# Kernel optimization log

Measured on AMD Instinct MI355X. Metric: run time of the kernel, lower is better.

## Reference

```python
import jax, jax.numpy as jnp
import numpy as np

N = 50000
E = 800000
D_IN = 128
D_OUT = 128
LN_EPS = 1e-5
DROP_P = 0.1


def setup_inputs() -> dict:
    key = jax.random.key(0)
    ks = jax.random.split(key, 8)
    x = jax.random.normal(ks[0], (N, D_IN), dtype=jnp.float32)
    edge_index = jax.random.randint(ks[1], (2, E), 0, N, dtype=jnp.int64)
    # dropout mask: binary keep-mask scaled by 1/(1-p), as torch dropout produces
    u = jax.random.uniform(ks[2], (N, D_IN), dtype=jnp.float32)
    dropout_mask = (u > DROP_P).astype(jnp.float32) / (1.0 - DROP_P)
    # LayerNorm affine params
    gamma = jnp.ones((D_IN,), dtype=jnp.float32)
    beta = jnp.zeros((D_IN,), dtype=jnp.float32)
    # SAGEConv linears: lin_l (aggregated neighbors, with bias), lin_r (root, no bias)
    s = 1.0 / np.sqrt(D_IN)
    w_l = jax.random.uniform(ks[3], (D_OUT, D_IN), minval=-s, maxval=s, dtype=jnp.float32)
    b_l = jax.random.uniform(ks[4], (D_OUT,), minval=-s, maxval=s, dtype=jnp.float32)
    w_r = jax.random.uniform(ks[5], (D_OUT, D_IN), minval=-s, maxval=s, dtype=jnp.float32)
    return {"x": x, "edge_index": edge_index, "dropout_mask": dropout_mask,
            "gamma": gamma, "beta": beta, "w_l": w_l, "b_l": b_l, "w_r": w_r}


def reference(x, edge_index, dropout_mask, gamma, beta, w_l, b_l, w_r):
    # LayerNorm + ReLU + dropout mask
    mu = jnp.mean(x, axis=-1, keepdims=True)
    var = jnp.mean(jnp.square(x - mu), axis=-1, keepdims=True)
    h = (x - mu) * jax.lax.rsqrt(var + LN_EPS) * gamma + beta
    h = jax.nn.relu(h) * dropout_mask  # [N, D_IN]
    # SAGEConv: mean-aggregate source features into target nodes
    src = edge_index[0]
    dst = edge_index[1]
    msg = h[src]  # [E, D_IN] gathered messages
    agg = jax.ops.segment_sum(msg, dst, num_segments=N)  # [N, D_IN]
    deg = jax.ops.segment_sum(jnp.ones((E,), dtype=h.dtype), dst, num_segments=N)
    agg = agg / jnp.maximum(deg, 1.0)[:, None]
    # out = lin_l(agg) + lin_r(h)
    out = agg @ w_l.T + b_l + h @ w_r.T  # [N, D_OUT]
    return out
```

## Files before the change

### kernel.cpp

```cpp
#include <hip/hip_runtime.h>
#include <hip/hip_bf16.h>

#define N_NODES 50000
#define N_EDGES 800000
#define D 128
#define NB_PREP ((N_NODES + 255) / 256)
#define NB_GEMM ((N_NODES + 63) / 64)
#define EDGES_PER_GEMM_BLOCK 1024
#define CAP 64

typedef short bf16x8 __attribute__((ext_vector_type(8)));
typedef float f32x4 __attribute__((ext_vector_type(4)));

__device__ __forceinline__ unsigned int bf16u(float f) {
  __hip_bfloat16 b = __float2bfloat16(f);
  return (unsigned int)*reinterpret_cast<unsigned short*>(&b);
}

__global__ __launch_bounds__(256) void prep_kernel(
    const float* __restrict__ w_l, const float* __restrict__ w_r,
    unsigned int* __restrict__ wb, int* __restrict__ deg) {
  const int i = blockIdx.x * 256 + threadIdx.x;
  if (i < N_NODES) deg[i] = 0;
  if (i < 4096) {
    const int fid = i >> 6;
    const int l = i & 63;
    const int lm = l & 15;
    const int quad = l >> 4;
    const int sub = fid >> 2;
    const int ch = fid & 3;
    const float* srcw = (sub < 8) ? (w_l + (size_t)(sub * 16 + lm) * D)
                                  : (w_r + (size_t)((sub - 8) * 16 + lm) * D);
    const float4 a = *(const float4*)(srcw + ch * 32 + quad * 8);
    const float4 b = *(const float4*)(srcw + ch * 32 + quad * 8 + 4);
    uint4 v;
    v.x = (bf16u(a.y) << 16) | bf16u(a.x);
    v.y = (bf16u(a.w) << 16) | bf16u(a.z);
    v.z = (bf16u(b.y) << 16) | bf16u(b.x);
    v.w = (bf16u(b.w) << 16) | bf16u(b.z);
    ((uint4*)wb)[(size_t)fid * 64 + l] = v;
  }
}

__global__ __launch_bounds__(256, 4) void gemm_kernel(
    const float* __restrict__ x, const float* __restrict__ mask,
    const float* __restrict__ gamma, const float* __restrict__ beta,
    const unsigned int* __restrict__ wb, const float* __restrict__ b_l,
    unsigned int* __restrict__ gb, float* __restrict__ rp,
    const int* __restrict__ ei, int* __restrict__ deg,
    unsigned short* __restrict__ bucket) {
  const int t = threadIdx.x;
  const int w = t >> 6;
  const int l = t & 63;
  const int lm = l & 15;
  const int quad = l >> 4;
  const int nb = blockIdx.x * 64;

  const int e = blockIdx.x * EDGES_PER_GEMM_BLOCK + t * 4;
  const bool efull = (e + 3 < N_EDGES);
  int4 d4, s4, r4;
  if (efull) {
    d4 = *(const int4*)(ei + N_EDGES + e);
    s4 = *(const int4*)(ei + e);
    r4.x = atomicAdd(&deg[d4.x], 1);
    r4.y = atomicAdd(&deg[d4.y], 1);
    r4.z = atomicAdd(&deg[d4.z], 1);
    r4.w = atomicAdd(&deg[d4.w], 1);
  } else {
    for (int k = e; k < N_EDGES; ++k) {
      const int dst = ei[N_EDGES + k];
      const int r = atomicAdd(&deg[dst], 1);
      if (r < CAP) bucket[(size_t)dst * CAP + r] = (unsigned short)ei[k];
    }
  }

  int anode = nb + w * 16 + lm;
  if (anode >= N_NODES) anode = N_NODES - 1;
  const float* xrow = x + (size_t)anode * D;
  float xv[32];
  float s = 0.f, q = 0.f;
#pragma unroll
  for (int ch = 0; ch < 4; ++ch) {
    const float4 a = *(const float4*)(xrow + ch * 32 + quad * 8);
    const float4 b = *(const float4*)(xrow + ch * 32 + quad * 8 + 4);
    xv[ch * 8 + 0] = a.x; xv[ch * 8 + 1] = a.y;
    xv[ch * 8 + 2] = a.z; xv[ch * 8 + 3] = a.w;
    xv[ch * 8 + 4] = b.x; xv[ch * 8 + 5] = b.y;
    xv[ch * 8 + 6] = b.z; xv[ch * 8 + 7] = b.w;
    s += (a.x + a.y) + (a.z + a.w) + (b.x + b.y) + (b.z + b.w);
    q += a.x * a.x + a.y * a.y + a.z * a.z + a.w * a.w +
         b.x * b.x + b.y * b.y + b.z * b.z + b.w * b.w;
  }
  s += __shfl_xor(s, 16);
  s += __shfl_xor(s, 32);
  q += __shfl_xor(q, 16);
  q += __shfl_xor(q, 32);
  const float mean = s * (1.0f / 128.0f);
  const float var = q * (1.0f / 128.0f) - mean * mean;
  const float rs = rsqrtf(var + 1e-5f);

  const float* mrow = mask + (size_t)anode * D;
  bf16x8 af[4];
#pragma unroll
  for (int ch = 0; ch < 4; ++ch) {
    const int c0 = ch * 32 + quad * 8;
    const float4 g0 = *(const float4*)(gamma + c0);
    const float4 g1 = *(const float4*)(gamma + c0 + 4);
    const float4 b0 = *(const float4*)(beta + c0);
    const float4 b1 = *(const float4*)(beta + c0 + 4);
    const float4 m0 = *(const float4*)(mrow + c0);
    const float4 m1 = *(const float4*)(mrow + c0 + 4);
    const float gv[8] = {g0.x, g0.y, g0.z, g0.w, g1.x, g1.y, g1.z, g1.w};
    const float bv[8] = {b0.x, b0.y, b0.z, b0.w, b1.x, b1.y, b1.z, b1.w};
    const float mv[8] = {m0.x, m0.y, m0.z, m0.w, m1.x, m1.y, m1.z, m1.w};
#pragma unroll
    for (int j = 0; j < 8; ++j) {
      const float hv =
          fmaxf((xv[ch * 8 + j] - mean) * rs * gv[j] + bv[j], 0.0f) * mv[j];
      af[ch][j] = (short)bf16u(hv);
    }
  }

  if (efull) {
    if (r4.x < CAP) bucket[(size_t)d4.x * CAP + r4.x] = (unsigned short)s4.x;
    if (r4.y < CAP) bucket[(size_t)d4.y * CAP + r4.y] = (unsigned short)s4.y;
    if (r4.z < CAP) bucket[(size_t)d4.z * CAP + r4.z] = (unsigned short)s4.z;
    if (r4.w < CAP) bucket[(size_t)d4.w * CAP + r4.w] = (unsigned short)s4.w;
  }

  f32x4 acc[16];
#pragma unroll
  for (int sub = 0; sub < 16; ++sub) acc[sub] = (f32x4){0.f, 0.f, 0.f, 0.f};
  const bf16x8* BsF = (const bf16x8*)wb;
#pragma unroll
  for (int sub = 0; sub < 16; ++sub)
#pragma unroll
    for (int ch = 0; ch < 4; ++ch)
      acc[sub] = __builtin_amdgcn_mfma_f32_16x16x32_bf16(
          af[ch], BsF[(sub * 4 + ch) * 64 + l], acc[sub], 0, 0, 0);

  float blv[8];
#pragma unroll
  for (int j = 0; j < 8; ++j) blv[j] = b_l[j * 16 + lm];

  const int node0 = nb + w * 16 + quad * 4;
#pragma unroll
  for (int reg = 0; reg < 4; ++reg) {
    const int node = node0 + reg;
    if (node < N_NODES) {
      uint4 p;
      p.x = (bf16u(acc[1][reg]) << 16) | bf16u(acc[0][reg]);
      p.y = (bf16u(acc[3][reg]) << 16) | bf16u(acc[2][reg]);
      p.z = (bf16u(acc[5][reg]) << 16) | bf16u(acc[4][reg]);
      p.w = (bf16u(acc[7][reg]) << 16) | bf16u(acc[6][reg]);
      ((uint4*)gb)[(size_t)node * 16 + lm] = p;
      float4 q0, q1;
      q0.x = acc[8][reg] + blv[0];
      q0.y = acc[9][reg] + blv[1];
      q0.z = acc[10][reg] + blv[2];
      q0.w = acc[11][reg] + blv[3];
      q1.x = acc[12][reg] + blv[4];
      q1.y = acc[13][reg] + blv[5];
      q1.z = acc[14][reg] + blv[6];
      q1.w = acc[15][reg] + blv[7];
      ((float4*)rp)[(size_t)node * 32 + lm * 2 + 0] = q0;
      ((float4*)rp)[(size_t)node * 32 + lm * 2 + 1] = q1;
    }
  }
}

#define ACC8(v)                                     \
  do {                                              \
    acc[0] += __uint_as_float((v).x << 16);         \
    acc[1] += __uint_as_float((v).x & 0xffff0000u); \
    acc[2] += __uint_as_float((v).y << 16);         \
    acc[3] += __uint_as_float((v).y & 0xffff0000u); \
    acc[4] += __uint_as_float((v).z << 16);         \
    acc[5] += __uint_as_float((v).z & 0xffff0000u); \
    acc[6] += __uint_as_float((v).w << 16);         \
    acc[7] += __uint_as_float((v).w & 0xffff0000u); \
  } while (0)

__global__ __launch_bounds__(256) void agg_kernel(
    const int* __restrict__ deg, const unsigned short* __restrict__ bucket,
    const unsigned int* __restrict__ gb, const float* __restrict__ rp,
    float* __restrict__ out) {
  const int l = threadIdx.x & 63;
  const int q = l >> 4;
  const int c = l & 15;
  const int n = blockIdx.x * 4 + (threadIdx.x >> 6);
  const int dg = deg[n];
  const int cnt = min(dg, CAP);
  const uint4* g4 = (const uint4*)gb;
  float acc[8];
#pragma unroll
  for (int k = 0; k < 8; ++k) acc[k] = 0.0f;
  int idx = (l < cnt) ? (int)bucket[(size_t)n * CAP + l] : 0;
  int j = 0;
  for (; j + 16 <= cnt; j += 16) {
    const int i0 = __shfl(idx, j + 0 + q);
    const int i1 = __shfl(idx, j + 4 + q);
    const int i2 = __shfl(idx, j + 8 + q);
    const int i3 = __shfl(idx, j + 12 + q);
    const uint4 v0 = g4[(size_t)i0 * 16 + c];
    const uint4 v1 = g4[(size_t)i1 * 16 + c];
    const uint4 v2 = g4[(size_t)i2 * 16 + c];
    const uint4 v3 = g4[(size_t)i3 * 16 + c];
    ACC8(v0);
    ACC8(v1);
    ACC8(v2);
    ACC8(v3);
  }
  for (; j + 4 <= cnt; j += 4) {
    const int i0 = __shfl(idx, j + q);
    const uint4 v0 = g4[(size_t)i0 * 16 + c];
    ACC8(v0);
  }
  if (j < cnt) {
    const int rem = cnt - j;
    const int i0 = __shfl(idx, j + min(q, rem - 1));
    if (q < rem) {
      const uint4 v0 = g4[(size_t)i0 * 16 + c];
      ACC8(v0);
    }
  }
#pragma unroll
  for (int k = 0; k < 8; ++k) {
    acc[k] += __shfl_xor(acc[k], 16);
    acc[k] += __shfl_xor(acc[k], 32);
  }
  if (l < 16) {
    const float inv = 1.0f / fmaxf((float)dg, 1.0f);
    const float4 rp0 = ((const float4*)rp)[(size_t)n * 32 + c * 2 + 0];
    const float4 rp1 = ((const float4*)rp)[(size_t)n * 32 + c * 2 + 1];
    float* o = out + (size_t)n * D + c;
    o[0]   = fmaf(acc[0], inv, rp0.x);
    o[16]  = fmaf(acc[1], inv, rp0.y);
    o[32]  = fmaf(acc[2], inv, rp0.z);
    o[48]  = fmaf(acc[3], inv, rp0.w);
    o[64]  = fmaf(acc[4], inv, rp1.x);
    o[80]  = fmaf(acc[5], inv, rp1.y);
    o[96]  = fmaf(acc[6], inv, rp1.z);
    o[112] = fmaf(acc[7], inv, rp1.w);
  }
}

extern "C" void kernel_launch(void* const* d_in, const int* in_sizes, int n_in,
                              void* d_out, int out_size, void* d_ws,
                              size_t ws_size, hipStream_t stream) {
  const float* x = (const float*)d_in[0];
  const int* ei = (const int*)d_in[1];
  const float* mask = (const float*)d_in[2];
  const float* gamma = (const float*)d_in[3];
  const float* beta = (const float*)d_in[4];
  const float* w_l = (const float*)d_in[5];
  const float* b_l = (const float*)d_in[6];
  const float* w_r = (const float*)d_in[7];
  float* out = (float*)d_out;

  char* ws = (char*)d_ws;
  size_t off = 0;
  auto alloc = [&](size_t bytes) {
    char* p = ws + off;
    off += (bytes + 255) & ~(size_t)255;
    return p;
  };
  unsigned int* gb =
      (unsigned int*)alloc((size_t)N_NODES * D * sizeof(unsigned short));
  float* rp = (float*)alloc((size_t)N_NODES * D * sizeof(float));
  int* deg = (int*)alloc((size_t)N_NODES * sizeof(int));
  unsigned short* bucket =
      (unsigned short*)alloc((size_t)N_NODES * CAP * sizeof(unsigned short));
  unsigned int* wb = (unsigned int*)alloc((size_t)4096 * 16);

  prep_kernel<<<NB_PREP, 256, 0, stream>>>(w_l, w_r, wb, deg);
  gemm_kernel<<<NB_GEMM, 256, 0, stream>>>(x, mask, gamma, beta, wb, b_l, gb,
                                           rp, ei, deg, bucket);
  agg_kernel<<<N_NODES / 4, 256, 0, stream>>>(deg, bucket, gb, rp, out);
}
```

Baseline: 222.8 us.

## Split GEMM output columns across wave pairs to halve accumulators and raise occupancy

Each GEMM block now handles 32 nodes instead of 64. Pairs of waves share the same 16 rows, with one wave computing the neighbor-projection half and the other the root-projection half. This halves the MFMA accumulator registers per wave, which allows a higher launch-bounds occupancy (6 waves per SIMD hint) and doubles the grid size. Edge bucketing per thread drops from 4 to 2 edges, and the tail loop is removed because the edge count divides evenly. The trade-off is that LayerNorm and the x/mask loads are now computed redundantly by both waves in each pair.

```diff
diff --git a/kernel.cpp b/kernel.cpp
--- a/kernel.cpp
+++ b/kernel.cpp
@@ -5,8 +5,8 @@
 #define N_EDGES 800000
 #define D 128
 #define NB_PREP ((N_NODES + 255) / 256)
-#define NB_GEMM ((N_NODES + 63) / 64)
-#define EDGES_PER_GEMM_BLOCK 1024
+#define NB_GEMM ((N_NODES + 31) / 32)
+#define EDGES_PER_GEMM_BLOCK 512
 #define CAP 64
 
 typedef short bf16x8 __attribute__((ext_vector_type(8)));
@@ -42,7 +42,7 @@
   }
 }
 
-__global__ __launch_bounds__(256, 4) void gemm_kernel(
+__global__ __launch_bounds__(256, 6) void gemm_kernel(
     const float* __restrict__ x, const float* __restrict__ mask,
     const float* __restrict__ gamma, const float* __restrict__ beta,
     const unsigned int* __restrict__ wb, const float* __restrict__ b_l,
@@ -54,27 +54,22 @@
   const int l = t & 63;
   const int lm = l & 15;
   const int quad = l >> 4;
-  const int nb = blockIdx.x * 64;
-
-  const int e = blockIdx.x * EDGES_PER_GEMM_BLOCK + t * 4;
-  const bool efull = (e + 3 < N_EDGES);
-  int4 d4, s4, r4;
+  const int half = w & 1;
+  const int rowg = w >> 1;
+  const int nb = blockIdx.x * 32;
+
+  const int e0 = blockIdx.x * EDGES_PER_GEMM_BLOCK + t * 2;
+  const bool efull = (e0 + 1 < N_EDGES);
+  int2 d2, s2;
+  int r0, r1;
   if (efull) {
-    d4 = *(const int4*)(ei + N_EDGES + e);
-    s4 = *(const int4*)(ei + e);
-    r4.x = atomicAdd(&deg[d4.x], 1);
-    r4.y = atomicAdd(&deg[d4.y], 1);
-    r4.z = atomicAdd(&deg[d4.z], 1);
-    r4.w = atomicAdd(&deg[d4.w], 1);
-  } else {
-    for (int k = e; k < N_EDGES; ++k) {
-      const int dst = ei[N_EDGES + k];
-      const int r = atomicAdd(&deg[dst], 1);
-      if (r < CAP) bucket[(size_t)dst * CAP + r] = (unsigned short)ei[k];
-    }
-  }
-
-  int anode = nb + w * 16 + lm;
+    d2 = *(const int2*)(ei + N_EDGES + e0);
+    s2 = *(const int2*)(ei + e0);
+    r0 = atomicAdd(&deg[d2.x], 1);
+    r1 = atomicAdd(&deg[d2.y], 1);
+  }
+
+  int anode = nb + rowg * 16 + lm;
   if (anode >= N_NODES) anode = N_NODES - 1;
   const float* xrow = x + (size_t)anode * D;
   float xv[32];
@@ -122,49 +117,57 @@
   }
 
   if (efull) {
-    if (r4.x < CAP) bucket[(size_t)d4.x * CAP + r4.x] = (unsigned short)s4.x;
-    if (r4.y < CAP) bucket[(size_t)d4.y * CAP + r4.y] = (unsigned short)s4.y;
-    if (r4.z < CAP) bucket[(size_t)d4.z * CAP + r4.z] = (unsigned short)s4.z;
-    if (r4.w < CAP) bucket[(size_t)d4.w * CAP + r4.w] = (unsigned short)s4.w;
-  }
-
-  f32x4 acc[16];
-#pragma unroll
-  for (int sub = 0; sub < 16; ++sub) acc[sub] = (f32x4){0.f, 0.f, 0.f, 0.f};
+    if (r0 < CAP) bucket[(size_t)d2.x * CAP + r0] = (unsigned short)s2.x;
+    if (r1 < CAP) bucket[(size_t)d2.y * CAP + r1] = (unsigned short)s2.y;
+  }
+
+  f32x4 acc[8];
+#pragma unroll
+  for (int sub = 0; sub < 8; ++sub) acc[sub] = (f32x4){0.f, 0.f, 0.f, 0.f};
   const bf16x8* BsF = (const bf16x8*)wb;
 #pragma unroll
-  for (int sub = 0; sub < 16; ++sub)
+  for (int sub = 0; sub < 8; ++sub) {
+    const int gsub = half * 8 + sub;
 #pragma unroll
     for (int ch = 0; ch < 4; ++ch)
       acc[sub] = __builtin_amdgcn_mfma_f32_16x16x32_bf16(
-          af[ch], BsF[(sub * 4 + ch) * 64 + l], acc[sub], 0, 0, 0);
-
-  float blv[8];
-#pragma unroll
-  for (int j = 0; j < 8; ++j) blv[j] = b_l[j * 16 + lm];
-
-  const int node0 = nb + w * 16 + quad * 4;
-#pragma unroll
-  for (int reg = 0; reg < 4; ++reg) {
-    const int node = node0 + reg;
-    if (node < N_NODES) {
-      uint4 p;
-      p.x = (bf16u(acc[1][reg]) << 16) | bf16u(acc[0][reg]);
-      p.y = (bf16u(acc[3][reg]) << 16) | bf16u(acc[2][reg]);
-      p.z = (bf16u(acc[5][reg]) << 16) | bf16u(acc[4][reg]);
-      p.w = (bf16u(acc[7][reg]) << 16) | bf16u(acc[6][reg]);
-      ((uint4*)gb)[(size_t)node * 16 + lm] = p;
-      float4 q0, q1;
-      q0.x = acc[8][reg] + blv[0];
-      q0.y = acc[9][reg] + blv[1];
-      q0.z = acc[10][reg] + blv[2];
-      q0.w = acc[11][reg] + blv[3];
-      q1.x = acc[12][reg] + blv[4];
-      q1.y = acc[13][reg] + blv[5];
-      q1.z = acc[14][reg] + blv[6];
-      q1.w = acc[15][reg] + blv[7];
-      ((float4*)rp)[(size_t)node * 32 + lm * 2 + 0] = q0;
-      ((float4*)rp)[(size_t)node * 32 + lm * 2 + 1] = q1;
+          af[ch], BsF[(gsub * 4 + ch) * 64 + l], acc[sub], 0, 0, 0);
+  }
+
+  const int node0 = nb + rowg * 16 + quad * 4;
+  if (half == 0) {
+#pragma unroll
+    for (int reg = 0; reg < 4; ++reg) {
+      const int node = node0 + reg;
+      if (node < N_NODES) {
+        uint4 p;
+        p.x = (bf16u(acc[1][reg]) << 16) | bf16u(acc[0][reg]);
+        p.y = (bf16u(acc[3][reg]) << 16) | bf16u(acc[2][reg]);
+        p.z = (bf16u(acc[5][reg]) << 16) | bf16u(acc[4][reg]);
+        p.w = (bf16u(acc[7][reg]) << 16) | bf16u(acc[6][reg]);
+        ((uint4*)gb)[(size_t)node * 16 + lm] = p;
+      }
+    }
+  } else {
+    float blv[8];
+#pragma unroll
+    for (int j = 0; j < 8; ++j) blv[j] = b_l[j * 16 + lm];
+#pragma unroll
+    for (int reg = 0; reg < 4; ++reg) {
+      const int node = node0 + reg;
+      if (node < N_NODES) {
+        float4 q0, q1;
+        q0.x = acc[0][reg] + blv[0];
+        q0.y = acc[1][reg] + blv[1];
+        q0.z = acc[2][reg] + blv[2];
+        q0.w = acc[3][reg] + blv[3];
+        q1.x = acc[4][reg] + blv[4];
+        q1.y = acc[5][reg] + blv[5];
+        q1.z = acc[6][reg] + blv[6];
+        q1.w = acc[7][reg] + blv[7];
+        ((float4*)rp)[(size_t)node * 32 + lm * 2 + 0] = q0;
+        ((float4*)rp)[(size_t)node * 32 + lm * 2 + 1] = q1;
+      }
     }
   }
 }
```

Result: slower. 264.9 us (+18.9%).

## Slice aggregation by feature column chunks across four passes for cache locality

Applied to the files above, without the earlier changes.

The aggregation kernel is split into four feature slices, each covering 4 of the 16 uint4 chunks of a node's bf16 row, launched as separate groups of blocks. Each wave now processes 16 edges per iteration with 4 lanes per edge, so each slice's gathered working set (a quarter of the gb table) fits better in cache. Nontemporal loads and stores are used for bucket, rp and out to avoid polluting cache. The cost is four reads of the bucket and deg per node, less memory-level parallelism per wave, and partial-line gathers of 64 bytes per row.

```diff
diff --git a/kernel.cpp b/kernel.cpp
--- a/kernel.cpp
+++ b/kernel.cpp
@@ -8,6 +8,8 @@
 #define NB_GEMM ((N_NODES + 63) / 64)
 #define EDGES_PER_GEMM_BLOCK 1024
 #define CAP 64
+#define SLICE_BLOCKS ((N_NODES + 3) / 4)
+#define NB_AGG (SLICE_BLOCKS * 4)
 
 typedef short bf16x8 __attribute__((ext_vector_type(8)));
 typedef float f32x4 __attribute__((ext_vector_type(4)));
@@ -169,79 +171,71 @@
   }
 }
 
-#define ACC8(v)                                     \
-  do {                                              \
-    acc[0] += __uint_as_float((v).x << 16);         \
-    acc[1] += __uint_as_float((v).x & 0xffff0000u); \
-    acc[2] += __uint_as_float((v).y << 16);         \
-    acc[3] += __uint_as_float((v).y & 0xffff0000u); \
-    acc[4] += __uint_as_float((v).z << 16);         \
-    acc[5] += __uint_as_float((v).z & 0xffff0000u); \
-    acc[6] += __uint_as_float((v).w << 16);         \
-    acc[7] += __uint_as_float((v).w & 0xffff0000u); \
-  } while (0)
-
 __global__ __launch_bounds__(256) void agg_kernel(
     const int* __restrict__ deg, const unsigned short* __restrict__ bucket,
     const unsigned int* __restrict__ gb, const float* __restrict__ rp,
     float* __restrict__ out) {
+  const int bid = blockIdx.x;
+  const int s = bid / SLICE_BLOCKS;
+  const int nb = bid - s * SLICE_BLOCKS;
+  const int w = threadIdx.x >> 6;
   const int l = threadIdx.x & 63;
-  const int q = l >> 4;
-  const int c = l & 15;
-  const int n = blockIdx.x * 4 + (threadIdx.x >> 6);
+  const int g = l >> 2;
+  const int c = l & 3;
+  const int chunk = s * 4 + c;
+  const int n = nb * 4 + w;
+  if (n >= N_NODES) return;
+
   const int dg = deg[n];
   const int cnt = min(dg, CAP);
+  int idx = 0;
+  if (l < cnt)
+    idx = (int)__builtin_nontemporal_load(bucket + (size_t)n * CAP + l);
+
   const uint4* g4 = (const uint4*)gb;
   float acc[8];
 #pragma unroll
   for (int k = 0; k < 8; ++k) acc[k] = 0.0f;
-  int idx = (l < cnt) ? (int)bucket[(size_t)n * CAP + l] : 0;
-  int j = 0;
-  for (; j + 16 <= cnt; j += 16) {
-    const int i0 = __shfl(idx, j + 0 + q);
-    const int i1 = __shfl(idx, j + 4 + q);
-    const int i2 = __shfl(idx, j + 8 + q);
-    const int i3 = __shfl(idx, j + 12 + q);
-    const uint4 v0 = g4[(size_t)i0 * 16 + c];
-    const uint4 v1 = g4[(size_t)i1 * 16 + c];
-    const uint4 v2 = g4[(size_t)i2 * 16 + c];
-    const uint4 v3 = g4[(size_t)i3 * 16 + c];
-    ACC8(v0);
-    ACC8(v1);
-    ACC8(v2);
-    ACC8(v3);
-  }
-  for (; j + 4 <= cnt; j += 4) {
-    const int i0 = __shfl(idx, j + q);
-    const uint4 v0 = g4[(size_t)i0 * 16 + c];
-    ACC8(v0);
-  }
-  if (j < cnt) {
-    const int rem = cnt - j;
-    const int i0 = __shfl(idx, j + min(q, rem - 1));
-    if (q < rem) {
-      const uint4 v0 = g4[(size_t)i0 * 16 + c];
-      ACC8(v0);
-    }
-  }
+
+  for (int base = 0; base < cnt; base += 16) {
+    const int e = base + g;
+    const int src = __shfl(idx, min(e, cnt - 1));
+    const uint4 v = g4[(size_t)src * 16 + chunk];
+    if (e < cnt) {
+      acc[0] += __uint_as_float(v.x << 16);
+      acc[1] += __uint_as_float(v.x & 0xffff0000u);
+      acc[2] += __uint_as_float(v.y << 16);
+      acc[3] += __uint_as_float(v.y & 0xffff0000u);
+      acc[4] += __uint_as_float(v.z << 16);
+      acc[5] += __uint_as_float(v.z & 0xffff0000u);
+      acc[6] += __uint_as_float(v.w << 16);
+      acc[7] += __uint_as_float(v.w & 0xffff0000u);
+    }
+  }
+
 #pragma unroll
   for (int k = 0; k < 8; ++k) {
+    acc[k] += __shfl_xor(acc[k], 4);
+    acc[k] += __shfl_xor(acc[k], 8);
     acc[k] += __shfl_xor(acc[k], 16);
     acc[k] += __shfl_xor(acc[k], 32);
   }
-  if (l < 16) {
+
+  if (l < 4) {
     const float inv = 1.0f / fmaxf((float)dg, 1.0f);
-    const float4 rp0 = ((const float4*)rp)[(size_t)n * 32 + c * 2 + 0];
-    const float4 rp1 = ((const float4*)rp)[(size_t)n * 32 + c * 2 + 1];
-    float* o = out + (size_t)n * D + c;
-    o[0]   = fmaf(acc[0], inv, rp0.x);
-    o[16]  = fmaf(acc[1], inv, rp0.y);
-    o[32]  = fmaf(acc[2], inv, rp0.z);
-    o[48]  = fmaf(acc[3], inv, rp0.w);
-    o[64]  = fmaf(acc[4], inv, rp1.x);
-    o[80]  = fmaf(acc[5], inv, rp1.y);
-    o[96]  = fmaf(acc[6], inv, rp1.z);
-    o[112] = fmaf(acc[7], inv, rp1.w);
+    const f32x4 r0 = __builtin_nontemporal_load(
+        (const f32x4*)rp + (size_t)n * 32 + chunk * 2);
+    const f32x4 r1 = __builtin_nontemporal_load(
+        (const f32x4*)rp + (size_t)n * 32 + chunk * 2 + 1);
+    float* o = out + (size_t)n * D + chunk;
+    __builtin_nontemporal_store(fmaf(acc[0], inv, r0.x), o);
+    __builtin_nontemporal_store(fmaf(acc[1], inv, r0.y), o + 16);
+    __builtin_nontemporal_store(fmaf(acc[2], inv, r0.z), o + 32);
+    __builtin_nontemporal_store(fmaf(acc[3], inv, r0.w), o + 48);
+    __builtin_nontemporal_store(fmaf(acc[4], inv, r1.x), o + 64);
+    __builtin_nontemporal_store(fmaf(acc[5], inv, r1.y), o + 80);
+    __builtin_nontemporal_store(fmaf(acc[6], inv, r1.z), o + 96);
+    __builtin_nontemporal_store(fmaf(acc[7], inv, r1.w), o + 112);
   }
 }
 
@@ -276,5 +270,5 @@
   prep_kernel<<<NB_PREP, 256, 0, stream>>>(w_l, w_r, wb, deg);
   gemm_kernel<<<NB_GEMM, 256, 0, stream>>>(x, mask, gamma, beta, wb, b_l, gb,
                                            rp, ei, deg, bucket);
-  agg_kernel<<<N_NODES / 4, 256, 0, stream>>>(deg, bucket, gb, rp, out);
-}
+  agg_kernel<<<NB_AGG, 256, 0, stream>>>(deg, bucket, gb, rp, out);
+}
```

Result: slower. 277.6 us (+24.6%).
